# Kernel tuning notes

Hardware: AMD Instinct MI355X
Metric: run time of the kernel (lower is better)

## Reference

```python
import jax, jax.numpy as jnp
from jax import lax
import numpy as np
import math

NUM_CLASSES = 81
N_PER_IMG = 1024
NUM_IMAGES = 8
SCORE_THRESH = 0.05
NMS_THRESH = 0.5
DETS_PER_IMG = 100
WX, WY, WW, WH = 10.0, 10.0, 5.0, 5.0
BBOX_XFORM_CLIP = math.log(1000.0 / 16.0)


def setup_inputs() -> dict:
    key = jax.random.key(0)
    k1, k2, k3, k4 = jax.random.split(key, 4)
    M = NUM_IMAGES * N_PER_IMG
    H, W = 800, 1333
    class_logits = jax.random.normal(k1, (M, NUM_CLASSES), dtype=jnp.float32) * 3.0
    box_regression = jax.random.normal(k2, (M, 4 * NUM_CLASSES), dtype=jnp.float32) * 0.5
    # valid xyxy proposals inside the image
    xy1 = jax.random.uniform(k3, (M, 2), dtype=jnp.float32) * jnp.array([W * 0.7, H * 0.7], jnp.float32)
    wh = jax.random.uniform(k4, (M, 2), dtype=jnp.float32) * jnp.array([W * 0.3, H * 0.3], jnp.float32) + 4.0
    proposals = jnp.concatenate([xy1, xy1 + wh], axis=1)
    return {"class_logits": class_logits, "box_regression": box_regression,
            "proposals": proposals, "height": H, "width": W}


def _decode(rel_codes, boxes):
    widths = boxes[:, 2] - boxes[:, 0] + 1.0
    heights = boxes[:, 3] - boxes[:, 1] + 1.0
    ctr_x = boxes[:, 0] + 0.5 * widths
    ctr_y = boxes[:, 1] + 0.5 * heights
    rel = rel_codes.reshape(rel_codes.shape[0], -1, 4)  # [M, C, 4]
    dx = rel[:, :, 0] / WX
    dy = rel[:, :, 1] / WY
    dw = jnp.minimum(rel[:, :, 2] / WW, BBOX_XFORM_CLIP)
    dh = jnp.minimum(rel[:, :, 3] / WH, BBOX_XFORM_CLIP)
    pctr_x = dx * widths[:, None] + ctr_x[:, None]
    pctr_y = dy * heights[:, None] + ctr_y[:, None]
    pw = jnp.exp(dw) * widths[:, None]
    ph = jnp.exp(dh) * heights[:, None]
    return jnp.stack([pctr_x - 0.5 * pw, pctr_y - 0.5 * ph,
                      pctr_x + 0.5 * pw - 1.0, pctr_y + 0.5 * ph - 1.0], axis=-1)


def _clip(boxes, height, width):
    # boxes [..., 4] xyxy, clamp to [0, W-1] x [0, H-1]
    x = jnp.clip(boxes[..., 0::2], 0.0, float(width - 1))
    y = jnp.clip(boxes[..., 1::2], 0.0, float(height - 1))
    return jnp.stack([x[..., 0], y[..., 0], x[..., 1], y[..., 1]], axis=-1)


def _iou_matrix(b):
    x1, y1, x2, y2 = b[:, 0], b[:, 1], b[:, 2], b[:, 3]
    area = (x2 - x1 + 1.0) * (y2 - y1 + 1.0)
    xx1 = jnp.maximum(x1[:, None], x1[None, :])
    yy1 = jnp.maximum(y1[:, None], y1[None, :])
    xx2 = jnp.minimum(x2[:, None], x2[None, :])
    yy2 = jnp.minimum(y2[:, None], y2[None, :])
    inter = jnp.clip(xx2 - xx1 + 1.0, 0.0) * jnp.clip(yy2 - yy1 + 1.0, 0.0)
    return inter / (area[:, None] + area[None, :] - inter)


def _per_class(scores_j, boxes_j):
    # scores_j [N], boxes_j [N,4] -> sorted scores/boxes + greedy-NMS keep mask
    N = scores_j.shape[0]
    valid = scores_j > SCORE_THRESH
    s = jnp.where(valid, scores_j, 0.0)  # softmax scores are > 0
    order = jnp.argsort(-s)
    s_sorted = s[order]
    b_sorted = boxes_j[order]
    valid_sorted = valid[order]
    iou = _iou_matrix(b_sorted)  # [N, N]
    idxs = jnp.arange(N)

    def body(i, keep):
        sup = (iou[i] > NMS_THRESH) & keep[i] & (idxs > i)
        return keep & ~sup

    keep = lax.fori_loop(0, N, body, valid_sorted)
    return s_sorted, b_sorted, keep


def _per_image(prob_i, boxes_i):
    # prob_i [N, C], boxes_i [N, C, 4]; skip background class 0
    C = prob_i.shape[1]
    fg_scores = prob_i[:, 1:].T                      # [C-1, N]
    fg_boxes = jnp.swapaxes(boxes_i[:, 1:, :], 0, 1)  # [C-1, N, 4]
    s_sorted, b_sorted, keep = jax.vmap(_per_class)(fg_scores, fg_boxes)
    labels = jnp.broadcast_to(jnp.arange(1, C, dtype=jnp.int32)[:, None], s_sorted.shape)
    flat_s = jnp.where(keep, s_sorted, 0.0).reshape(-1)
    vals, idx = lax.top_k(flat_s, DETS_PER_IMG)      # detections-per-image limit
    boxes_out = b_sorted.reshape(-1, 4)[idx]
    labels_out = labels.reshape(-1)[idx]
    ok = vals > SCORE_THRESH
    return (jnp.where(ok, vals, 0.0),
            jnp.where(ok[:, None], boxes_out, 0.0),
            jnp.where(ok, labels_out, 0))


def reference(class_logits, box_regression, proposals, height, width):
    prob = jax.nn.softmax(class_logits, axis=-1)          # [M, C]
    dec = _decode(box_regression, proposals)              # [M, C, 4]
    dec = _clip(dec, height, width)
    B, N, C = NUM_IMAGES, N_PER_IMG, NUM_CLASSES
    prob = prob.reshape(B, N, C)
    dec = dec.reshape(B, N, C, 4)
    scores, boxes, labels = lax.map(lambda a: _per_image(a[0], a[1]), (prob, dec))
    return scores, boxes, labels
```

## Files before the change

### kernel.cpp

```cpp
#include <hip/hip_runtime.h>
#include <stdint.h>
#include <math.h>

#define NCLS 81
#define NFG  80
#define NPI  1024
#define NIMG 8
#define DETS 100
#define SCORE_T 0.05f
#define NMS_T   0.5f
#define NCAND   (NFG * DETS)
#define CAND_CAP 1024
#define ROWS 64

static constexpr float BBOX_CLIP = 4.1351665567423557f;

__device__ __forceinline__ float rlf(float v, int i) {
#if __has_builtin(__builtin_amdgcn_readlane)
    return __uint_as_float((unsigned)__builtin_amdgcn_readlane((int)__float_as_uint(v), i));
#else
    return __shfl(v, i, 64);
#endif
}

__global__ __launch_bounds__(256) void softmax_probT(
    const float* __restrict__ logits, float* __restrict__ probT, int M)
{
    __shared__ float tile[ROWS * NCLS];
    __shared__ float mx[ROWS], dn[ROWS];
    int t = threadIdx.x;
    int rbase = blockIdx.x * ROWS;
    for (int idx = t; idx < ROWS * NCLS; idx += 256)
        tile[idx] = logits[(size_t)rbase * NCLS + idx];
    __syncthreads();
    if (t < ROWS) {
        const float* r = tile + t * NCLS;
        float m = r[0];
        #pragma unroll
        for (int j = 1; j < NCLS; ++j) m = fmaxf(m, r[j]);
        float s = 0.f;
        #pragma unroll
        for (int j = 0; j < NCLS; ++j) s += expf(r[j] - m);
        mx[t] = m; dn[t] = s;
    }
    __syncthreads();
    for (int o = t; o < ROWS * NFG; o += 256) {
        int r = o & 63;
        int c = o >> 6;
        probT[(size_t)c * M + rbase + r] = expf(tile[r * NCLS + (c + 1)] - mx[r]) / dn[r];
    }
}

__global__ __launch_bounds__(64) void per_class_nms(
    const float* __restrict__ probT, const float* __restrict__ boxreg,
    const float* __restrict__ props, const int* __restrict__ hptr,
    const int* __restrict__ wptr, int* __restrict__ out_cnt,
    float* __restrict__ out_score, unsigned* __restrict__ out_key,
    float* __restrict__ out_box, int M)
{
    int pid = blockIdx.x;
    int img = pid / NFG;
    int c   = pid % NFG;
    int cls = c + 1;
    int lane = threadIdx.x;

    __shared__ unsigned long long pkey[NPI];
    __shared__ unsigned long long skey[NPI];
    __shared__ float pbox[NPI][4];
    __shared__ unsigned long long remv[16];

    float W1 = (float)(*wptr - 1);
    float H1 = (float)(*hptr - 1);

    int cnt = 0;
    const float* pT = probT + (size_t)c * M + img * NPI;

    #pragma unroll
    for (int it = 0; it < NPI / 256; ++it) {
        float4 pv = *(const float4*)(pT + it * 256 + lane * 4);
        float pr[4] = {pv.x, pv.y, pv.z, pv.w};
        #pragma unroll
        for (int j = 0; j < 4; ++j) {
            bool pass = pr[j] > SCORE_T;
            unsigned long long bal = __ballot(pass);
            if (pass) {
                int m = it * 256 + lane * 4 + j;
                int g = img * NPI + m;
                int mypos = cnt + __popcll(bal & ((1ULL << lane) - 1ULL));
                const float4 pb = *(const float4*)(props + (size_t)g * 4);
                float x1 = pb.x, y1 = pb.y, x2 = pb.z, y2 = pb.w;
                float w  = x2 - x1 + 1.0f, h = y2 - y1 + 1.0f;
                float cx = x1 + 0.5f * w,  cy = y1 + 0.5f * h;
                const float4 rc = *(const float4*)(boxreg + (size_t)g * (4 * NCLS) + 4 * cls);
                float dx = rc.x / 10.0f, dy = rc.y / 10.0f;
                float dw = fminf(rc.z / 5.0f, BBOX_CLIP);
                float dh = fminf(rc.w / 5.0f, BBOX_CLIP);
                float pcx = dx * w + cx, pcy = dy * h + cy;
                float pw = expf(dw) * w, ph = expf(dh) * h;
                float bx1 = fminf(fmaxf(pcx - 0.5f * pw, 0.f), W1);
                float by1 = fminf(fmaxf(pcy - 0.5f * ph, 0.f), H1);
                float bx2 = fminf(fmaxf(pcx + 0.5f * pw - 1.0f, 0.f), W1);
                float by2 = fminf(fmaxf(pcy + 0.5f * ph - 1.0f, 0.f), H1);
                pbox[mypos][0] = bx1; pbox[mypos][1] = by1;
                pbox[mypos][2] = bx2; pbox[mypos][3] = by2;
                pkey[mypos] = ((unsigned long long)__float_as_uint(pr[j]) << 32)
                            | ((unsigned)(NPI - 1 - m) << 10) | (unsigned)mypos;
            }
            cnt += __popcll(bal);
        }
    }
    int n = cnt;
    __syncthreads();

    if (n <= 64) {
        unsigned long long k = (lane < n) ? pkey[lane] : 0ULL;
        #pragma unroll
        for (int kk = 2; kk <= 64; kk <<= 1) {
            #pragma unroll
            for (int j = kk >> 1; j > 0; j >>= 1) {
                unsigned long long o = __shfl_xor(k, j, 64);
                bool take_max = (((lane & kk) == 0) == ((lane & j) == 0));
                k = take_max ? (k > o ? k : o) : (k < o ? k : o);
            }
        }
        bool valid = (lane < n);
        float bx1 = 0.f, by1 = 0.f, bx2 = 0.f, by2 = 0.f, area = 0.f;
        if (valid) {
            int pos = (int)(k & 0x3FFu);
            bx1 = pbox[pos][0]; by1 = pbox[pos][1];
            bx2 = pbox[pos][2]; by2 = pbox[pos][3];
            area = (bx2 - bx1 + 1.f) * (by2 - by1 + 1.f);
        }
        unsigned long long sup = 0ULL;
        for (int i = 0; i < n; ++i) {
            if ((sup >> i) & 1ULL) continue;
            float ax1 = rlf(bx1, i), ay1 = rlf(by1, i);
            float ax2 = rlf(bx2, i), ay2 = rlf(by2, i);
            float aarea = rlf(area, i);
            bool s = false;
            if (valid && lane > i) {
                float xx1 = fmaxf(ax1, bx1), yy1 = fmaxf(ay1, by1);
                float xx2 = fminf(ax2, bx2), yy2 = fminf(ay2, by2);
                float iw = fmaxf(xx2 - xx1 + 1.f, 0.f);
                float ih = fmaxf(yy2 - yy1 + 1.f, 0.f);
                float inter = iw * ih;
                s = inter / (aarea + area - inter) > NMS_T;
            }
            sup |= __ballot(s);
        }
        bool kept = valid && !((sup >> lane) & 1ULL);
        unsigned long long keptm = __ballot(kept);
        int rank = __popcll(keptm & ((1ULL << lane) - 1ULL));
        if (kept && rank < DETS) {
            int slot = pid * DETS + rank;
            out_score[slot] = __uint_as_float((unsigned)(k >> 32));
            out_key[slot] = (unsigned)(c * NPI + lane);
            out_box[slot * 4 + 0] = bx1; out_box[slot * 4 + 1] = by1;
            out_box[slot * 4 + 2] = bx2; out_box[slot * 4 + 3] = by2;
        }
        if (lane == 0) {
            int tot = __popcll(keptm);
            out_cnt[pid] = tot < DETS ? tot : DETS;
        }
        return;
    }

    for (int i = lane; i < n; i += 64) {
        unsigned long long ki = pkey[i];
        int r = 0;
        for (int j = 0; j < n; ++j) r += (pkey[j] > ki) ? 1 : 0;
        skey[r] = ki;
    }
    if (lane < 16) remv[lane] = 0ULL;
    __syncthreads();

    int nch = (n + 63) >> 6;
    for (int a = 0; a < nch; ++a) {
        int ea = a * 64 + lane;
        bool va = ea < n;
        float bx1 = 0.f, by1 = 0.f, bx2 = 0.f, by2 = 0.f, area = 0.f;
        if (va) {
            int pos = (int)(skey[ea] & 0x3FFu);
            bx1 = pbox[pos][0]; by1 = pbox[pos][1];
            bx2 = pbox[pos][2]; by2 = pbox[pos][3];
            area = (bx2 - bx1 + 1.f) * (by2 - by1 + 1.f);
        }
        unsigned long long sup = remv[a];
        int lim = (n - a * 64 < 64) ? (n - a * 64) : 64;
        for (int i = 0; i < lim; ++i) {
            if ((sup >> i) & 1ULL) continue;
            float ax1 = rlf(bx1, i), ay1 = rlf(by1, i);
            float ax2 = rlf(bx2, i), ay2 = rlf(by2, i);
            float aarea = rlf(area, i);
            bool s = false;
            if (va && lane > i) {
                float xx1 = fmaxf(ax1, bx1), yy1 = fmaxf(ay1, by1);
                float xx2 = fminf(ax2, bx2), yy2 = fminf(ay2, by2);
                float iw = fmaxf(xx2 - xx1 + 1.f, 0.f);
                float ih = fmaxf(yy2 - yy1 + 1.f, 0.f);
                float inter = iw * ih;
                s = inter / (aarea + area - inter) > NMS_T;
            }
            sup |= __ballot(s);
        }
        if (lane == 0) remv[a] = sup;
        for (int b = a + 1; b < nch; ++b) {
            int eb = b * 64 + lane;
            bool vb = eb < n;
            float cx1 = 0.f, cy1 = 0.f, cx2 = 0.f, cy2 = 0.f, carea = 0.f;
            if (vb) {
                int pos = (int)(skey[eb] & 0x3FFu);
                cx1 = pbox[pos][0]; cy1 = pbox[pos][1];
                cx2 = pbox[pos][2]; cy2 = pbox[pos][3];
                carea = (cx2 - cx1 + 1.f) * (cy2 - cy1 + 1.f);
            }
            unsigned long long supb = 0ULL;
            for (int i = 0; i < lim; ++i) {
                if ((sup >> i) & 1ULL) continue;
                float ax1 = rlf(bx1, i), ay1 = rlf(by1, i);
                float ax2 = rlf(bx2, i), ay2 = rlf(by2, i);
                float aarea = rlf(area, i);
                bool s = false;
                if (vb) {
                    float xx1 = fmaxf(ax1, cx1), yy1 = fmaxf(ay1, cy1);
                    float xx2 = fminf(ax2, cx2), yy2 = fminf(ay2, cy2);
                    float iw = fmaxf(xx2 - xx1 + 1.f, 0.f);
                    float ih = fmaxf(yy2 - yy1 + 1.f, 0.f);
                    float inter = iw * ih;
                    s = inter / (aarea + carea - inter) > NMS_T;
                }
                supb |= __ballot(s);
            }
            if (lane == 0) remv[b] |= supb;
            __syncthreads();
        }
        __syncthreads();
    }

    unsigned long long vmasks[16];
    int base[17];
    base[0] = 0;
    for (int ch = 0; ch < nch; ++ch) {
        int rem = n - ch * 64;
        unsigned long long vm = (rem >= 64) ? ~0ULL : ((1ULL << rem) - 1ULL);
        vmasks[ch] = vm;
        base[ch + 1] = base[ch] + __popcll(~remv[ch] & vm);
    }
    for (int e = lane; e < n; e += 64) {
        int ch = e >> 6;
        unsigned long long rm = remv[ch];
        bool kept = !((rm >> (e & 63)) & 1ULL);
        if (kept) {
            int r = base[ch] + __popcll(~rm & vmasks[ch] & ((1ULL << (e & 63)) - 1ULL));
            if (r < DETS) {
                unsigned long long ki = skey[e];
                int pos = (int)(ki & 0x3FFu);
                int slot = pid * DETS + r;
                out_score[slot] = __uint_as_float((unsigned)(ki >> 32));
                out_key[slot] = (unsigned)(c * NPI + e);
                out_box[slot * 4 + 0] = pbox[pos][0];
                out_box[slot * 4 + 1] = pbox[pos][1];
                out_box[slot * 4 + 2] = pbox[pos][2];
                out_box[slot * 4 + 3] = pbox[pos][3];
            }
        }
    }
    if (lane == 0) {
        int tot = base[nch];
        out_cnt[pid] = tot < DETS ? tot : DETS;
    }
}

__device__ __forceinline__ void suffix_select256(
    unsigned* hist, unsigned* wtot, int K, int* outB, unsigned* outAbove)
{
    int t = threadIdx.x, lane = t & 63, w = t >> 6;
    unsigned loc[16]; unsigned ps = 0;
    #pragma unroll
    for (int j = 0; j < 16; ++j) { loc[j] = hist[t * 16 + j]; ps += loc[j]; }
    unsigned v = ps;
    #pragma unroll
    for (int off = 1; off < 64; off <<= 1) {
        unsigned u = __shfl_down(v, off, 64);
        v += (lane + off < 64) ? u : 0u;
    }
    if (lane == 0) wtot[w] = v;
    __syncthreads();
    unsigned woff = 0;
    for (int w2 = w + 1; w2 < 4; ++w2) woff += wtot[w2];
    unsigned base = v + woff - ps;
    unsigned suf = 0;
    #pragma unroll
    for (int j = 15; j >= 0; --j) {
        unsigned A = base + suf;
        if ((int)A < K && (int)(A + loc[j]) >= K) { *outB = t * 16 + j; *outAbove = A; }
        suf += loc[j];
    }
    __syncthreads();
}

__global__ __launch_bounds__(256) void topk_merge(
    const int* __restrict__ cnts, const float* __restrict__ escore,
    const unsigned* __restrict__ ekey, const float* __restrict__ ebox,
    float* __restrict__ out)
{
    int img = blockIdx.x;
    __shared__ unsigned sc[NCAND];
    __shared__ unsigned hist[4096];
    __shared__ unsigned long long cand[CAND_CAP];
    __shared__ int scnts[NFG];
    __shared__ unsigned wtot[4];
    __shared__ int sB1, sB2, sNc;
    __shared__ unsigned sAb1, sAb2;

    int t = threadIdx.x;
    if (t < NFG) scnts[t] = cnts[img * NFG + t];
    if (t == 0) { sB1 = 0; sB2 = 0; sNc = 0; sAb1 = 0; sAb2 = 0; }
    for (int i = t; i < 4096; i += 256) hist[i] = 0;
    __syncthreads();

    for (int p = t; p < NCAND; p += 256) {
        unsigned fb = 0;
        if ((p % DETS) < scnts[p / DETS]) fb = __float_as_uint(escore[img * NCAND + p]);
        sc[p] = fb;
        if (fb) atomicAdd(&hist[fb >> 19], 1u);
    }
    __syncthreads();
    suffix_select256(hist, wtot, DETS, &sB1, &sAb1);
    int B1 = sB1; unsigned ab1 = sAb1;

    for (int i = t; i < 4096; i += 256) hist[i] = 0;
    __syncthreads();
    for (int p = t; p < NCAND; p += 256) {
        unsigned fb = sc[p];
        if (fb && (int)(fb >> 19) == B1) atomicAdd(&hist[(fb >> 7) & 0xFFFu], 1u);
    }
    __syncthreads();
    suffix_select256(hist, wtot, DETS - (int)ab1, &sB2, &sAb2);
    int B2 = sB2;

    for (int p = t; p < NCAND; p += 256) {
        unsigned fb = sc[p];
        if (fb) {
            int d1 = (int)(fb >> 19);
            bool ok = d1 > B1 || (d1 == B1 && (int)((fb >> 7) & 0xFFFu) >= B2);
            if (ok) {
                int pos = atomicAdd(&sNc, 1);
                if (pos < CAND_CAP) {
                    unsigned fk = ekey[img * NCAND + p];
                    cand[pos] = ((unsigned long long)fb << 32)
                              | (((0x1FFFFu - fk) << 13) | (unsigned)p);
                }
            }
        }
    }
    __syncthreads();
    int nc = sNc < CAND_CAP ? sNc : CAND_CAP;

    float* oScore = out;
    float* oBox   = out + NIMG * DETS;
    float* oLab   = out + NIMG * DETS * 5;

    for (int k = t; k < DETS; k += 256) {
        if (k >= nc) {
            int o = img * DETS + k;
            oScore[o] = 0.f;
            oBox[o * 4 + 0] = 0.f; oBox[o * 4 + 1] = 0.f;
            oBox[o * 4 + 2] = 0.f; oBox[o * 4 + 3] = 0.f;
            oLab[o] = 0.f;
        }
    }

    for (int i = t; i < nc; i += 256) {
        unsigned long long ki = cand[i];
        int r = 0;
        for (int j = 0; j < nc; ++j) r += (cand[j] > ki) ? 1 : 0;
        if (r < DETS) {
            float scv = __uint_as_float((unsigned)(ki >> 32));
            unsigned low = (unsigned)(ki & 0xFFFFFFFFu);
            unsigned flatkey = 0x1FFFFu - ((low >> 13) & 0x1FFFFu);
            int p = (int)(low & 0x1FFFu);
            int gp = img * NCAND + p;
            int o = img * DETS + r;
            oScore[o] = scv;
            oBox[o * 4 + 0] = ebox[gp * 4 + 0];
            oBox[o * 4 + 1] = ebox[gp * 4 + 1];
            oBox[o * 4 + 2] = ebox[gp * 4 + 2];
            oBox[o * 4 + 3] = ebox[gp * 4 + 3];
            oLab[o] = (float)((flatkey >> 10) + 1);
        }
    }
}

extern "C" void kernel_launch(void* const* d_in, const int* in_sizes, int n_in,
                              void* d_out, int out_size, void* d_ws, size_t ws_size,
                              hipStream_t stream) {
    const float* logits = (const float*)d_in[0];
    const float* boxreg = (const float*)d_in[1];
    const float* props  = (const float*)d_in[2];
    const int*   hptr   = (const int*)d_in[3];
    const int*   wptr   = (const int*)d_in[4];
    float* out = (float*)d_out;
    int M = in_sizes[0] / NCLS;

    char* ws = (char*)d_ws;
    float*    probT  = (float*)ws;    ws += (size_t)NFG * M * sizeof(float);
    int*      gcnt   = (int*)ws;      ws += (size_t)NIMG * NFG * sizeof(int);
    float*    escore = (float*)ws;    ws += (size_t)NIMG * NCAND * sizeof(float);
    unsigned* ekey   = (unsigned*)ws; ws += (size_t)NIMG * NCAND * sizeof(unsigned);
    float*    ebox   = (float*)ws;    ws += (size_t)NIMG * NCAND * 4 * sizeof(float);

    softmax_probT<<<M / ROWS, 256, 0, stream>>>(logits, probT, M);
    per_class_nms<<<NIMG * NFG, 64, 0, stream>>>(
        probT, boxreg, props, hptr, wptr, gcnt, escore, ekey, ebox, M);
    topk_merge<<<NIMG, 256, 0, stream>>>(gcnt, escore, ekey, ebox, out);
}
```

Before: 71.74 us.

## Fuse decode and score filtering into softmax kernel; pack four NMS classes per block

Score filtering and box decoding move into the softmax kernel, which appends passing candidates to per-(image,class) global buckets through atomics, so the transposed probability buffer is no longer written. NMS then runs one wavefront per class, four per 256-thread block, reading keys and boxes from global memory and using wave-local fences instead of block barriers. This cuts the full probT write/read and the per-class rescanning of all 1024 probabilities. In exchange it adds a memset and atomic contention, and candidate order now depends on atomic ordering; the 64-bit keys (score, then proposal index) still give a deterministic sort. The __threadfence_block only acts as a wave-local sync because each wave works on its own LDS slots, and lane 0's LDS writes are visible to the other lanes of the same wave.

Result: slower. 116.3 us (+62.1%).

```diff
diff --git a/kernel.cpp b/kernel.cpp
--- a/kernel.cpp
+++ b/kernel.cpp
@@ -12,6 +12,7 @@
 #define NCAND   (NFG * DETS)
 #define CAND_CAP 1024
 #define ROWS 64
+#define NPID (NIMG * NFG)
 
 static constexpr float BBOX_CLIP = 4.1351665567423557f;
 
@@ -23,13 +24,17 @@
 #endif
 }
 
-__global__ __launch_bounds__(256) void softmax_probT(
-    const float* __restrict__ logits, float* __restrict__ probT, int M)
+__global__ __launch_bounds__(256) void decode_filter(
+    const float* __restrict__ logits, const float* __restrict__ boxreg,
+    const float* __restrict__ props, const int* __restrict__ hptr,
+    const int* __restrict__ wptr, int* __restrict__ cnt,
+    unsigned long long* __restrict__ key8, float4* __restrict__ box16, int M)
 {
     __shared__ float tile[ROWS * NCLS];
     __shared__ float mx[ROWS], dn[ROWS];
     int t = threadIdx.x;
     int rbase = blockIdx.x * ROWS;
+
     for (int idx = t; idx < ROWS * NCLS; idx += 256)
         tile[idx] = logits[(size_t)rbase * NCLS + idx];
     __syncthreads();
@@ -44,91 +49,79 @@
         mx[t] = m; dn[t] = s;
     }
     __syncthreads();
-    for (int o = t; o < ROWS * NFG; o += 256) {
-        int r = o & 63;
-        int c = o >> 6;
-        probT[(size_t)c * M + rbase + r] = expf(tile[r * NCLS + (c + 1)] - mx[r]) / dn[r];
-    }
-}
-
-__global__ __launch_bounds__(64) void per_class_nms(
-    const float* __restrict__ probT, const float* __restrict__ boxreg,
-    const float* __restrict__ props, const int* __restrict__ hptr,
-    const int* __restrict__ wptr, int* __restrict__ out_cnt,
-    float* __restrict__ out_score, unsigned* __restrict__ out_key,
-    float* __restrict__ out_box, int M)
-{
-    int pid = blockIdx.x;
-    int img = pid / NFG;
-    int c   = pid % NFG;
-    int cls = c + 1;
-    int lane = threadIdx.x;
-
-    __shared__ unsigned long long pkey[NPI];
-    __shared__ unsigned long long skey[NPI];
-    __shared__ float pbox[NPI][4];
-    __shared__ unsigned long long remv[16];
 
     float W1 = (float)(*wptr - 1);
     float H1 = (float)(*hptr - 1);
 
-    int cnt = 0;
-    const float* pT = probT + (size_t)c * M + img * NPI;
-
-    #pragma unroll
-    for (int it = 0; it < NPI / 256; ++it) {
-        float4 pv = *(const float4*)(pT + it * 256 + lane * 4);
-        float pr[4] = {pv.x, pv.y, pv.z, pv.w};
+    for (int o = t; o < ROWS * NFG; o += 256) {
+        int r  = o & 63;
+        int cc = o >> 6;
+        float pr = expf(tile[r * NCLS + (cc + 1)] - mx[r]) / dn[r];
+        if (pr > SCORE_T) {
+            int row = rbase + r;
+            int img = row >> 10;
+            int m   = row & 1023;
+            int pid = img * NFG + cc;
+            int cls = cc + 1;
+            const float4 pb = *(const float4*)(props + (size_t)row * 4);
+            float x1 = pb.x, y1 = pb.y, x2 = pb.z, y2 = pb.w;
+            float w  = x2 - x1 + 1.0f, h = y2 - y1 + 1.0f;
+            float cx = x1 + 0.5f * w,  cy = y1 + 0.5f * h;
+            const float4 rc = *(const float4*)(boxreg + (size_t)row * (4 * NCLS) + 4 * cls);
+            float dx = rc.x / 10.0f, dy = rc.y / 10.0f;
+            float dw = fminf(rc.z / 5.0f, BBOX_CLIP);
+            float dh = fminf(rc.w / 5.0f, BBOX_CLIP);
+            float pcx = dx * w + cx, pcy = dy * h + cy;
+            float pw = expf(dw) * w, ph = expf(dh) * h;
+            float bx1 = fminf(fmaxf(pcx - 0.5f * pw, 0.f), W1);
+            float by1 = fminf(fmaxf(pcy - 0.5f * ph, 0.f), H1);
+            float bx2 = fminf(fmaxf(pcx + 0.5f * pw - 1.0f, 0.f), W1);
+            float by2 = fminf(fmaxf(pcy + 0.5f * ph - 1.0f, 0.f), H1);
+            int pos = atomicAdd(&cnt[pid], 1);
+            key8[(size_t)pid * CAND_CAP + pos] =
+                ((unsigned long long)__float_as_uint(pr) << 32)
+              | ((unsigned)(NPI - 1 - m) << 10) | (unsigned)pos;
+            box16[(size_t)pid * CAND_CAP + pos] = make_float4(bx1, by1, bx2, by2);
+        }
+    }
+}
+
+__global__ __launch_bounds__(256) void wave_nms(
+    const int* __restrict__ cnt, const unsigned long long* __restrict__ key8,
+    const float4* __restrict__ box16, int* __restrict__ out_cnt,
+    float* __restrict__ out_score, unsigned* __restrict__ out_key,
+    float* __restrict__ out_box)
+{
+    __shared__ unsigned long long skey_lds[4][CAND_CAP];
+    __shared__ unsigned long long remv_lds[4][16];
+    __shared__ int base_lds[4][17];
+
+    int wid  = threadIdx.x >> 6;
+    int lane = threadIdx.x & 63;
+    int pid  = blockIdx.x * 4 + wid;
+    int c    = pid % NFG;
+
+    int n = cnt[pid];
+    if (n > CAND_CAP) n = CAND_CAP;
+    const unsigned long long* kk = key8 + (size_t)pid * CAND_CAP;
+    const float4* bb = box16 + (size_t)pid * CAND_CAP;
+
+    if (n <= 64) {
+        unsigned long long k = (lane < n) ? kk[lane] : 0ULL;
         #pragma unroll
-        for (int j = 0; j < 4; ++j) {
-            bool pass = pr[j] > SCORE_T;
-            unsigned long long bal = __ballot(pass);
-            if (pass) {
-                int m = it * 256 + lane * 4 + j;
-                int g = img * NPI + m;
-                int mypos = cnt + __popcll(bal & ((1ULL << lane) - 1ULL));
-                const float4 pb = *(const float4*)(props + (size_t)g * 4);
-                float x1 = pb.x, y1 = pb.y, x2 = pb.z, y2 = pb.w;
-                float w  = x2 - x1 + 1.0f, h = y2 - y1 + 1.0f;
-                float cx = x1 + 0.5f * w,  cy = y1 + 0.5f * h;
-                const float4 rc = *(const float4*)(boxreg + (size_t)g * (4 * NCLS) + 4 * cls);
-                float dx = rc.x / 10.0f, dy = rc.y / 10.0f;
-                float dw = fminf(rc.z / 5.0f, BBOX_CLIP);
-                float dh = fminf(rc.w / 5.0f, BBOX_CLIP);
-                float pcx = dx * w + cx, pcy = dy * h + cy;
-                float pw = expf(dw) * w, ph = expf(dh) * h;
-                float bx1 = fminf(fmaxf(pcx - 0.5f * pw, 0.f), W1);
-                float by1 = fminf(fmaxf(pcy - 0.5f * ph, 0.f), H1);
-                float bx2 = fminf(fmaxf(pcx + 0.5f * pw - 1.0f, 0.f), W1);
-                float by2 = fminf(fmaxf(pcy + 0.5f * ph - 1.0f, 0.f), H1);
-                pbox[mypos][0] = bx1; pbox[mypos][1] = by1;
-                pbox[mypos][2] = bx2; pbox[mypos][3] = by2;
-                pkey[mypos] = ((unsigned long long)__float_as_uint(pr[j]) << 32)
-                            | ((unsigned)(NPI - 1 - m) << 10) | (unsigned)mypos;
-            }
-            cnt += __popcll(bal);
-        }
-    }
-    int n = cnt;
-    __syncthreads();
-
-    if (n <= 64) {
-        unsigned long long k = (lane < n) ? pkey[lane] : 0ULL;
-        #pragma unroll
-        for (int kk = 2; kk <= 64; kk <<= 1) {
+        for (int kk2 = 2; kk2 <= 64; kk2 <<= 1) {
             #pragma unroll
-            for (int j = kk >> 1; j > 0; j >>= 1) {
+            for (int j = kk2 >> 1; j > 0; j >>= 1) {
                 unsigned long long o = __shfl_xor(k, j, 64);
-                bool take_max = (((lane & kk) == 0) == ((lane & j) == 0));
+                bool take_max = (((lane & kk2) == 0) == ((lane & j) == 0));
                 k = take_max ? (k > o ? k : o) : (k < o ? k : o);
             }
         }
         bool valid = (lane < n);
         float bx1 = 0.f, by1 = 0.f, bx2 = 0.f, by2 = 0.f, area = 0.f;
         if (valid) {
-            int pos = (int)(k & 0x3FFu);
-            bx1 = pbox[pos][0]; by1 = pbox[pos][1];
-            bx2 = pbox[pos][2]; by2 = pbox[pos][3];
+            float4 b = bb[(int)(k & 0x3FFu)];
+            bx1 = b.x; by1 = b.y; bx2 = b.z; by2 = b.w;
             area = (bx2 - bx1 + 1.f) * (by2 - by1 + 1.f);
         }
         unsigned long long sup = 0ULL;
@@ -166,13 +159,13 @@
     }
 
     for (int i = lane; i < n; i += 64) {
-        unsigned long long ki = pkey[i];
+        unsigned long long ki = kk[i];
         int r = 0;
-        for (int j = 0; j < n; ++j) r += (pkey[j] > ki) ? 1 : 0;
-        skey[r] = ki;
-    }
-    if (lane < 16) remv[lane] = 0ULL;
-    __syncthreads();
+        for (int j = 0; j < n; ++j) r += (kk[j] > ki) ? 1 : 0;
+        skey_lds[wid][r] = ki;
+    }
+    if (lane < 16) remv_lds[wid][lane] = 0ULL;
+    __threadfence_block();
 
     int nch = (n + 63) >> 6;
     for (int a = 0; a < nch; ++a) {
@@ -180,12 +173,11 @@
         bool va = ea < n;
         float bx1 = 0.f, by1 = 0.f, bx2 = 0.f, by2 = 0.f, area = 0.f;
         if (va) {
-            int pos = (int)(skey[ea] & 0x3FFu);
-            bx1 = pbox[pos][0]; by1 = pbox[pos][1];
-            bx2 = pbox[pos][2]; by2 = pbox[pos][3];
+            float4 b = bb[(int)(skey_lds[wid][ea] & 0x3FFu)];
+            bx1 = b.x; by1 = b.y; bx2 = b.z; by2 = b.w;
             area = (bx2 - bx1 + 1.f) * (by2 - by1 + 1.f);
         }
-        unsigned long long sup = remv[a];
+        unsigned long long sup = remv_lds[wid][a];
         int lim = (n - a * 64 < 64) ? (n - a * 64) : 64;
         for (int i = 0; i < lim; ++i) {
             if ((sup >> i) & 1ULL) continue;
@@ -203,15 +195,14 @@
             }
             sup |= __ballot(s);
         }
-        if (lane == 0) remv[a] = sup;
-        for (int b = a + 1; b < nch; ++b) {
-            int eb = b * 64 + lane;
+        if (lane == 0) remv_lds[wid][a] = sup;
+        for (int b2 = a + 1; b2 < nch; ++b2) {
+            int eb = b2 * 64 + lane;
             bool vb = eb < n;
             float cx1 = 0.f, cy1 = 0.f, cx2 = 0.f, cy2 = 0.f, carea = 0.f;
             if (vb) {
-                int pos = (int)(skey[eb] & 0x3FFu);
-                cx1 = pbox[pos][0]; cy1 = pbox[pos][1];
-                cx2 = pbox[pos][2]; cy2 = pbox[pos][3];
+                float4 b = bb[(int)(skey_lds[wid][eb] & 0x3FFu)];
+                cx1 = b.x; cy1 = b.y; cx2 = b.z; cy2 = b.w;
                 carea = (cx2 - cx1 + 1.f) * (cy2 - cy1 + 1.f);
             }
             unsigned long long supb = 0ULL;
@@ -231,42 +222,44 @@
                 }
                 supb |= __ballot(s);
             }
-            if (lane == 0) remv[b] |= supb;
-            __syncthreads();
-        }
-        __syncthreads();
-    }
-
-    unsigned long long vmasks[16];
-    int base[17];
-    base[0] = 0;
-    for (int ch = 0; ch < nch; ++ch) {
+            if (lane == 0) remv_lds[wid][b2] |= supb;
+            __threadfence_block();
+        }
+        __threadfence_block();
+    }
+
+    if (lane == 0) {
+        base_lds[wid][0] = 0;
+        for (int ch = 0; ch < nch; ++ch) {
+            int rem = n - ch * 64;
+            unsigned long long vm = (rem >= 64) ? ~0ULL : ((1ULL << rem) - 1ULL);
+            base_lds[wid][ch + 1] = base_lds[wid][ch]
+                                  + __popcll(~remv_lds[wid][ch] & vm);
+        }
+    }
+    __threadfence_block();
+    for (int e = lane; e < n; e += 64) {
+        int ch = e >> 6;
+        unsigned long long rm = remv_lds[wid][ch];
         int rem = n - ch * 64;
         unsigned long long vm = (rem >= 64) ? ~0ULL : ((1ULL << rem) - 1ULL);
-        vmasks[ch] = vm;
-        base[ch + 1] = base[ch] + __popcll(~remv[ch] & vm);
-    }
-    for (int e = lane; e < n; e += 64) {
-        int ch = e >> 6;
-        unsigned long long rm = remv[ch];
         bool kept = !((rm >> (e & 63)) & 1ULL);
         if (kept) {
-            int r = base[ch] + __popcll(~rm & vmasks[ch] & ((1ULL << (e & 63)) - 1ULL));
+            int r = base_lds[wid][ch]
+                  + __popcll(~rm & vm & ((1ULL << (e & 63)) - 1ULL));
             if (r < DETS) {
-                unsigned long long ki = skey[e];
-                int pos = (int)(ki & 0x3FFu);
+                unsigned long long ki = skey_lds[wid][e];
+                float4 b = bb[(int)(ki & 0x3FFu)];
                 int slot = pid * DETS + r;
                 out_score[slot] = __uint_as_float((unsigned)(ki >> 32));
                 out_key[slot] = (unsigned)(c * NPI + e);
-                out_box[slot * 4 + 0] = pbox[pos][0];
-                out_box[slot * 4 + 1] = pbox[pos][1];
-                out_box[slot * 4 + 2] = pbox[pos][2];
-                out_box[slot * 4 + 3] = pbox[pos][3];
+                out_box[slot * 4 + 0] = b.x; out_box[slot * 4 + 1] = b.y;
+                out_box[slot * 4 + 2] = b.z; out_box[slot * 4 + 3] = b.w;
             }
         }
     }
     if (lane == 0) {
-        int tot = base[nch];
+        int tot = base_lds[wid][nch];
         out_cnt[pid] = tot < DETS ? tot : DETS;
     }
 }
@@ -404,14 +397,19 @@
     int M = in_sizes[0] / NCLS;
 
     char* ws = (char*)d_ws;
-    float*    probT  = (float*)ws;    ws += (size_t)NFG * M * sizeof(float);
-    int*      gcnt   = (int*)ws;      ws += (size_t)NIMG * NFG * sizeof(int);
-    float*    escore = (float*)ws;    ws += (size_t)NIMG * NCAND * sizeof(float);
-    unsigned* ekey   = (unsigned*)ws; ws += (size_t)NIMG * NCAND * sizeof(unsigned);
-    float*    ebox   = (float*)ws;    ws += (size_t)NIMG * NCAND * 4 * sizeof(float);
-
-    softmax_probT<<<M / ROWS, 256, 0, stream>>>(logits, probT, M);
-    per_class_nms<<<NIMG * NFG, 64, 0, stream>>>(
-        probT, boxreg, props, hptr, wptr, gcnt, escore, ekey, ebox, M);
+    int*                cnt    = (int*)ws;                 ws += (size_t)NPID * sizeof(int);
+    int*                gcnt   = (int*)ws;                 ws += (size_t)NPID * sizeof(int);
+    ws = (char*)(((uintptr_t)ws + 15) & ~(uintptr_t)15);
+    unsigned long long* key8   = (unsigned long long*)ws;  ws += (size_t)NPID * CAND_CAP * 8;
+    float4*             box16  = (float4*)ws;              ws += (size_t)NPID * CAND_CAP * 16;
+    float*              escore = (float*)ws;               ws += (size_t)NIMG * NCAND * sizeof(float);
+    unsigned*           ekey   = (unsigned*)ws;            ws += (size_t)NIMG * NCAND * sizeof(unsigned);
+    float*              ebox   = (float*)ws;               ws += (size_t)NIMG * NCAND * 4 * sizeof(float);
+
+    hipMemsetAsync(cnt, 0, (size_t)NPID * sizeof(int), stream);
+    decode_filter<<<M / ROWS, 256, 0, stream>>>(
+        logits, boxreg, props, hptr, wptr, cnt, key8, box16, M);
+    wave_nms<<<NPID / 4, 256, 0, stream>>>(
+        cnt, key8, box16, gcnt, escore, ekey, ebox);
     topk_merge<<<NIMG, 256, 0, stream>>>(gcnt, escore, ekey, ebox, out);
 }
```
